# Performance work log

Measured on AMD Instinct MI355X. Metric: run time of the kernel, lower is better.

## Reference

```python
import jax, jax.numpy as jnp
import numpy as np

B, L, D = 1, 1024, 1024
NL = 4            # n_layers
N = 16            # d_state
DI = 2 * D        # d_inner (expand=2)
DTR = (D + 15) // 16  # dt_rank = ceil(d_model/16) = 64
K = 4             # depthwise conv kernel size
EPS = 1e-5


def setup_inputs() -> dict:
    key = jax.random.key(0)
    ks = jax.random.split(key, 8)
    s = lambda k, shp, sc: jax.random.normal(k, shp, jnp.float32) * sc
    x = s(ks[0], (B, L, D), 1.0)
    norm_w = jnp.ones((NL, D), jnp.float32)
    in_w = s(ks[1], (NL, 2 * DI, D), D ** -0.5)          # in_proj (no bias)
    conv_w = s(ks[2], (NL, DI, K), 0.5)                   # depthwise conv1d weight
    conv_b = s(ks[3], (NL, DI), 0.02)                     # conv1d bias
    xproj_w = s(ks[4], (NL, DTR + 2 * N, DI), DI ** -0.5) # x_proj (no bias)
    dt_w = s(ks[5], (NL, DI, DTR), DTR ** -0.5)           # dt_proj weight
    dt_b = jnp.full((NL, DI), 0.1, jnp.float32)           # dt_proj bias (positive-ish delta)
    A_log = jnp.log(jnp.tile(jnp.arange(1, N + 1, dtype=jnp.float32), (NL, DI, 1)))  # [NL, DI, N]
    D_skip = jnp.ones((NL, DI), jnp.float32)
    out_w = s(ks[6], (NL, D, DI), DI ** -0.5)             # out_proj (no bias)
    return dict(x=x, norm_w=norm_w, in_w=in_w, conv_w=conv_w, conv_b=conv_b,
                xproj_w=xproj_w, dt_w=dt_w, dt_b=dt_b, A_log=A_log,
                D_skip=D_skip, out_w=out_w)


def _rmsnorm(x, w):
    return x * jax.lax.rsqrt(jnp.mean(x * x, axis=-1, keepdims=True) + EPS) * w


def _causal_depthwise_conv(u, w, b):
    # u: [B, L, DI], w: [DI, K], b: [DI]; causal (left pad K-1)
    up = jnp.pad(u, ((0, 0), (K - 1, 0), (0, 0)))
    y = b
    for k in range(K):
        y = y + up[:, k:k + L, :] * w[:, k]
    return y


def _selective_scan(dA, dBu, C):
    # dA, dBu: [B, L, DI, N]; C: [B, L, N]
    def step(h, inp):
        a, bu, c = inp
        h = a * h + bu                       # [B, DI, N]
        y = jnp.einsum('bdn,bn->bd', h, c)   # [B, DI]
        return h, y
    h0 = jnp.zeros((dA.shape[0], DI, N), dA.dtype)
    _, ys = jax.lax.scan(step, h0, (dA.transpose(1, 0, 2, 3),
                                    dBu.transpose(1, 0, 2, 3),
                                    C.transpose(1, 0, 2)))
    return ys.transpose(1, 0, 2)             # [B, L, DI]


def _mamba_block(x, p):
    norm_w, in_w, conv_w, conv_b, xproj_w, dt_w, dt_b, A_log, D_skip, out_w = p
    xn = _rmsnorm(x, norm_w)
    xz = jnp.einsum('bld,ed->ble', xn, in_w)             # [B, L, 2*DI]
    u, z = jnp.split(xz, 2, axis=-1)
    u = jax.nn.silu(_causal_depthwise_conv(u, conv_w, conv_b))
    x_dbl = jnp.einsum('bld,ed->ble', u, xproj_w)        # [B, L, DTR+2N]
    dt_r, Bt, Ct = jnp.split(x_dbl, [DTR, DTR + N], axis=-1)
    delta = jax.nn.softplus(jnp.einsum('blr,dr->bld', dt_r, dt_w) + dt_b)  # [B, L, DI]
    A = -jnp.exp(A_log)                                  # [DI, N]
    dA = jnp.exp(delta[..., None] * A)                   # [B, L, DI, N]
    dBu = delta[..., None] * Bt[:, :, None, :] * u[..., None]
    y = _selective_scan(dA, dBu, Ct) + u * D_skip        # [B, L, DI]
    y = y * jax.nn.silu(z)
    return x + jnp.einsum('ble,de->bld', y, out_w)       # residual


def reference(x, norm_w, in_w, conv_w, conv_b, xproj_w, dt_w, dt_b, A_log, D_skip, out_w):
    params = (norm_w, in_w, conv_w, conv_b, xproj_w, dt_w, dt_b, A_log, D_skip, out_w)
    out, _ = jax.lax.scan(lambda h, p: (_mamba_block(h, p), None), x, params)
    return out
```

## Files before the change

kernel.cpp:

```cpp
#include <hip/hip_runtime.h>
#include <hip/hip_bf16.h>
#include <stdint.h>

#define L 1024
#define D 1024
#define NLAYER 4
#define NSTATE 16
#define DI 2048
#define DTR 64
#define KCONV 4
#define XD 96
#define NC 64
#define CT 16
#define KSPLIT 8
#define BK 32
#define DIST 4

typedef __attribute__((ext_vector_type(8))) short short8;
typedef __attribute__((ext_vector_type(4))) float floatx4;

__device__ __forceinline__ float siluf(float x) { return x / (1.f + __expf(-x)); }

__device__ __forceinline__ unsigned short f2bf(float x) {
    __hip_bfloat16 b = __float2bfloat16(x);
    return *reinterpret_cast<unsigned short*>(&b);
}

__device__ __forceinline__ short8 pack8(floatx4 a, floatx4 b) {
    short8 o;
    o[0] = (short)f2bf(a.x); o[1] = (short)f2bf(a.y);
    o[2] = (short)f2bf(a.z); o[3] = (short)f2bf(a.w);
    o[4] = (short)f2bf(b.x); o[5] = (short)f2bf(b.y);
    o[6] = (short)f2bf(b.z); o[7] = (short)f2bf(b.w);
    return o;
}

#define BARRIER_NODRAIN() asm volatile("s_waitcnt lgkmcnt(0)\n\ts_barrier" ::: "memory")

__global__ __launch_bounds__(256) void rmsnorm_kernel(const float* __restrict__ x,
                                                      const float* __restrict__ w,
                                                      __hip_bfloat16* __restrict__ out) {
    int row = blockIdx.x;
    const float* xr = x + (size_t)row * D;
    float v[4];
    float s = 0.f;
#pragma unroll
    for (int i = 0; i < 4; ++i) {
        v[i] = xr[threadIdx.x + i * 256];
        s += v[i] * v[i];
    }
#pragma unroll
    for (int off = 32; off > 0; off >>= 1) s += __shfl_xor(s, off, 64);
    __shared__ float red[4];
    int wave = threadIdx.x >> 6;
    if ((threadIdx.x & 63) == 0) red[wave] = s;
    __syncthreads();
    float tot = red[0] + red[1] + red[2] + red[3];
    float inv = rsqrtf(tot * (1.f / D) + 1e-5f);
#pragma unroll
    for (int i = 0; i < 4; ++i) {
        int c = threadIdx.x + i * 256;
        out[(size_t)row * D + c] = __float2bfloat16(v[i] * inv * w[c]);
    }
}

template <int EPI, int ITERS>
__global__ __launch_bounds__(256, 2) void gemm_pipe(
    const __hip_bfloat16* __restrict__ A, int lda,
    const float* __restrict__ Bw, int ldb, int Brows,
    float* __restrict__ C, int ldc, int Nvalid,
    long zstride, const float* __restrict__ bias) {
    __shared__ __align__(16) __hip_bfloat16 As[2][128 * BK];
    __shared__ __align__(16) __hip_bfloat16 Bs[2][64 * BK];
    int tid = threadIdx.x;
    int wave = tid >> 6, lane = tid & 63;

    int gxy = gridDim.x * gridDim.y;
    int total = gxy * gridDim.z;
    int flat = (blockIdx.z * gridDim.y + blockIdx.y) * gridDim.x + blockIdx.x;
    int bm, bn, bz;
    if ((total & 7) == 0) {
        int lid = (flat & 7) * (total >> 3) + (flat >> 3);
        bz = lid / gxy;
        int rem = lid - bz * gxy;
        bn = rem / gridDim.y;
        bm = rem - bn * gridDim.y;
    } else {
        bm = blockIdx.y; bn = blockIdx.x; bz = blockIdx.z;
    }

    int m0 = bm * 128, n0 = bn * 64;
    int k_base = bz * (ITERS * BK);
    C += (long)bz * zstride;
    int wr = wave >> 1, wc = wave & 1;
    int srow = lane >> 2, scol = (lane & 3) * 8;
    int q = lane >> 4, r = lane & 15;

    floatx4 acc[4][2] = {};

    const __hip_bfloat16* gA0 = A + (long)(m0 + wave * 32 + srow) * lda + scol + k_base;
    const __hip_bfloat16* gA1 = gA0 + (long)16 * lda;
    int bnrow = n0 + wave * 16 + srow;
    const float* gB = Bw + (long)bnrow * ldb + scol + k_base;
    bool bok = bnrow < Brows;

    short8 qa0[DIST], qa1[DIST];
    floatx4 qb0[DIST] = {}, qb1[DIST] = {};

    auto ld = [&](int j) {
        int k0 = j * BK;
        int s = j & (DIST - 1);
        qa0[s] = *(const short8*)(gA0 + k0);
        qa1[s] = *(const short8*)(gA1 + k0);
        if (bok) {
            qb0[s] = *(const floatx4*)(gB + k0);
            qb1[s] = *(const floatx4*)(gB + k0 + 4);
        }
    };
    auto wrstage = [&](int j) {
        int p = j & 1, s = j & (DIST - 1);
        *(short8*)(&As[p][(wave * 32 + srow) * BK + scol]) = qa0[s];
        *(short8*)(&As[p][(wave * 32 + 16 + srow) * BK + scol]) = qa1[s];
        *(short8*)(&Bs[p][(wave * 16 + srow) * BK + scol]) = pack8(qb0[s], qb1[s]);
    };

#pragma unroll
    for (int j = 0; j < DIST; ++j)
        if (j < ITERS) ld(j);
    wrstage(0);

#pragma unroll
    for (int k = 0; k < ITERS; ++k) {
        BARRIER_NODRAIN();
        if (k + DIST < ITERS) ld(k + DIST);
        if (k + 1 < ITERS) wrstage(k + 1);
        const short* Ap = (const short*)As[k & 1];
        const short* Bp = (const short*)Bs[k & 1];
        short8 af[4], bfr[2];
#pragma unroll
        for (int i = 0; i < 4; ++i)
            af[i] = *(const short8*)(Ap + (wr * 64 + i * 16 + r) * BK + q * 8);
#pragma unroll
        for (int j = 0; j < 2; ++j)
            bfr[j] = *(const short8*)(Bp + (wc * 32 + j * 16 + r) * BK + q * 8);
#pragma unroll
        for (int i = 0; i < 4; ++i)
#pragma unroll
            for (int j = 0; j < 2; ++j)
                acc[i][j] = __builtin_amdgcn_mfma_f32_16x16x32_bf16(af[i], bfr[j], acc[i][j], 0, 0, 0);
    }

#pragma unroll
    for (int i = 0; i < 4; ++i) {
        int mrow = m0 + wr * 64 + i * 16 + q * 4;
#pragma unroll
        for (int j = 0; j < 2; ++j) {
            int ncol = n0 + wc * 32 + j * 16 + r;
            if (ncol < Nvalid) {
#pragma unroll
                for (int rr = 0; rr < 4; ++rr) {
                    float v = acc[i][j][rr];
                    int m = mrow + rr;
                    if (EPI == 1) {
                        v += bias[ncol];
                        v = v > 20.f ? v : log1pf(__expf(v));
                    }
                    C[(long)m * ldc + ncol] = v;
                }
            }
        }
    }
}

template <bool NORM>
__global__ __launch_bounds__(256) void reduce2_kernel(const float* __restrict__ part2,
                                                      const float* __restrict__ xin,
                                                      const float* __restrict__ nw,
                                                      float* __restrict__ out,
                                                      __hip_bfloat16* __restrict__ xn) {
    int row = blockIdx.x;
    const float* p0 = part2 + (size_t)row * D;
    const float* p1 = p0 + (size_t)L * D;
    const float* xr = xin + (size_t)row * D;
    float v[4];
    float ss = 0.f;
#pragma unroll
    for (int i = 0; i < 4; ++i) {
        int c = threadIdx.x + i * 256;
        v[i] = p0[c] + p1[c] + xr[c];
        out[(size_t)row * D + c] = v[i];
        ss += v[i] * v[i];
    }
    if (NORM) {
#pragma unroll
        for (int off = 32; off > 0; off >>= 1) ss += __shfl_xor(ss, off, 64);
        __shared__ float red[4];
        int wave = threadIdx.x >> 6;
        if ((threadIdx.x & 63) == 0) red[wave] = ss;
        __syncthreads();
        float inv = rsqrtf((red[0] + red[1] + red[2] + red[3]) * (1.f / D) + 1e-5f);
#pragma unroll
        for (int i = 0; i < 4; ++i) {
            int c = threadIdx.x + i * 256;
            xn[(size_t)row * D + c] = __float2bfloat16(v[i] * inv * nw[c]);
        }
    }
}

__global__ __launch_bounds__(256) void conv_silu_kernel(const float* __restrict__ xz,
                                                        const float* __restrict__ cw,
                                                        const float* __restrict__ cb,
                                                        __hip_bfloat16* __restrict__ u) {
    int idx = blockIdx.x * 256 + threadIdx.x;
    int d = idx & (DI - 1);
    int t = idx >> 11;
    float acc = cb[d];
#pragma unroll
    for (int k = 0; k < KCONV; ++k) {
        int tk = t - (KCONV - 1) + k;
        if (tk >= 0) acc += xz[(size_t)tk * (2 * DI) + d] * cw[d * KCONV + k];
    }
    u[idx] = __float2bfloat16(siluf(acc));
}

__global__ __launch_bounds__(256) void xred_kernel(const float* __restrict__ part,
                                                   __hip_bfloat16* __restrict__ xdbl_bf,
                                                   float* __restrict__ xdblBC) {
    int i = blockIdx.x * 256 + threadIdx.x;
    int t = i / XD, col = i - t * XD;
    float s = 0.f;
#pragma unroll
    for (int sp = 0; sp < KSPLIT; ++sp) s += part[(size_t)sp * L * XD + i];
    if (col < DTR) xdbl_bf[(size_t)t * DTR + col] = __float2bfloat16(s);
    else xdblBC[(size_t)t * 32 + (col - DTR)] = s;
}

__global__ __launch_bounds__(256) void scanA_kernel(const float* __restrict__ delta,
                                                    const __hip_bfloat16* __restrict__ u,
                                                    const float* __restrict__ xdblBC,
                                                    const float* __restrict__ Alog,
                                                    float* __restrict__ Ach,
                                                    float* __restrict__ Bch) {
    int d = blockIdx.x * 256 + threadIdx.x;
    int c = blockIdx.y;
    __shared__ __align__(16) float Bsh[CT * NSTATE];
    int tt0 = threadIdx.x >> 4, c0 = threadIdx.x & 15;
    Bsh[threadIdx.x] = xdblBC[(size_t)(c * CT + tt0) * 32 + c0];
    __syncthreads();

    float aval[NSTATE];
    const float4* Al4 = (const float4*)(Alog + (size_t)d * NSTATE);
#pragma unroll
    for (int n4 = 0; n4 < 4; ++n4) {
        float4 t = Al4[n4];
        aval[n4 * 4 + 0] = -__expf(t.x);
        aval[n4 * 4 + 1] = -__expf(t.y);
        aval[n4 * 4 + 2] = -__expf(t.z);
        aval[n4 * 4 + 3] = -__expf(t.w);
    }
    float h[NSTATE], ap[NSTATE];
#pragma unroll
    for (int n = 0; n < NSTATE; ++n) { h[n] = 0.f; ap[n] = 1.f; }

    for (int tt = 0; tt < CT; ++tt) {
        int t = c * CT + tt;
        float dl = delta[(size_t)t * DI + d];
        float uu = __bfloat162float(u[(size_t)t * DI + d]);
        float du = dl * uu;
        const float4* Bv = (const float4*)(Bsh + tt * NSTATE);
#pragma unroll
        for (int n4 = 0; n4 < 4; ++n4) {
            float4 b = Bv[n4];
            float bb[4] = {b.x, b.y, b.z, b.w};
#pragma unroll
            for (int k = 0; k < 4; ++k) {
                int n = n4 * 4 + k;
                float a = __expf(dl * aval[n]);
                h[n] = a * h[n] + du * bb[k];
                ap[n] *= a;
            }
        }
    }
    float4* Ao = (float4*)(Ach + ((size_t)c * DI + d) * NSTATE);
    float4* Bo = (float4*)(Bch + ((size_t)c * DI + d) * NSTATE);
#pragma unroll
    for (int n4 = 0; n4 < 4; ++n4) {
        Ao[n4] = make_float4(ap[n4 * 4], ap[n4 * 4 + 1], ap[n4 * 4 + 2], ap[n4 * 4 + 3]);
        Bo[n4] = make_float4(h[n4 * 4], h[n4 * 4 + 1], h[n4 * 4 + 2], h[n4 * 4 + 3]);
    }
}

__global__ __launch_bounds__(256) void scanB_kernel(float* __restrict__ Ach,
                                                    const float* __restrict__ Bch) {
    long i = blockIdx.x * 256 + threadIdx.x;
    const long S = (long)DI * NSTATE;
    float h = 0.f;
    for (int c = 0; c < NC; ++c) {
        float a = Ach[c * S + i];
        float b = Bch[c * S + i];
        Ach[c * S + i] = h;
        h = a * h + b;
    }
}

__global__ __launch_bounds__(256) void scanC_kernel(const float* __restrict__ delta,
                                                    const __hip_bfloat16* __restrict__ u,
                                                    const float* __restrict__ xdblBC,
                                                    const float* __restrict__ Alog,
                                                    const float* __restrict__ Hin,
                                                    const float* __restrict__ xz,
                                                    const float* __restrict__ Dskip,
                                                    __hip_bfloat16* __restrict__ yg) {
    int d = blockIdx.x * 256 + threadIdx.x;
    int c = blockIdx.y;
    __shared__ __align__(16) float Bsh[CT * NSTATE];
    __shared__ __align__(16) float Csh[CT * NSTATE];
    int tt0 = threadIdx.x >> 4, c0 = threadIdx.x & 15;
    Bsh[threadIdx.x] = xdblBC[(size_t)(c * CT + tt0) * 32 + c0];
    Csh[threadIdx.x] = xdblBC[(size_t)(c * CT + tt0) * 32 + 16 + c0];
    __syncthreads();

    float aval[NSTATE];
    const float4* Al4 = (const float4*)(Alog + (size_t)d * NSTATE);
#pragma unroll
    for (int n4 = 0; n4 < 4; ++n4) {
        float4 t = Al4[n4];
        aval[n4 * 4 + 0] = -__expf(t.x);
        aval[n4 * 4 + 1] = -__expf(t.y);
        aval[n4 * 4 + 2] = -__expf(t.z);
        aval[n4 * 4 + 3] = -__expf(t.w);
    }
    float h[NSTATE];
    const float4* Hi = (const float4*)(Hin + ((size_t)c * DI + d) * NSTATE);
#pragma unroll
    for (int n4 = 0; n4 < 4; ++n4) {
        float4 t = Hi[n4];
        h[n4 * 4 + 0] = t.x; h[n4 * 4 + 1] = t.y; h[n4 * 4 + 2] = t.z; h[n4 * 4 + 3] = t.w;
    }
    float dsk = Dskip[d];

    for (int tt = 0; tt < CT; ++tt) {
        int t = c * CT + tt;
        float dl = delta[(size_t)t * DI + d];
        float uu = __bfloat162float(u[(size_t)t * DI + d]);
        float du = dl * uu;
        const float4* Bv = (const float4*)(Bsh + tt * NSTATE);
        const float4* Cv = (const float4*)(Csh + tt * NSTATE);
        float y = 0.f;
#pragma unroll
        for (int n4 = 0; n4 < 4; ++n4) {
            float4 b = Bv[n4];
            float4 cc = Cv[n4];
            float bb[4] = {b.x, b.y, b.z, b.w};
            float cv[4] = {cc.x, cc.y, cc.z, cc.w};
#pragma unroll
            for (int k = 0; k < 4; ++k) {
                int n = n4 * 4 + k;
                float a = __expf(dl * aval[n]);
                h[n] = a * h[n] + du * bb[k];
                y += h[n] * cv[k];
            }
        }
        float z = xz[(size_t)t * (2 * DI) + DI + d];
        yg[(size_t)t * DI + d] = __float2bfloat16((y + uu * dsk) * siluf(z));
    }
}

extern "C" void kernel_launch(void* const* d_in, const int* in_sizes, int n_in,
                              void* d_out, int out_size, void* d_ws, size_t ws_size,
                              hipStream_t stream) {
    const float* x      = (const float*)d_in[0];
    const float* norm_w = (const float*)d_in[1];
    const float* in_w   = (const float*)d_in[2];
    const float* conv_w = (const float*)d_in[3];
    const float* conv_b = (const float*)d_in[4];
    const float* xproj_w= (const float*)d_in[5];
    const float* dt_w   = (const float*)d_in[6];
    const float* dt_b   = (const float*)d_in[7];
    const float* A_log  = (const float*)d_in[8];
    const float* D_skip = (const float*)d_in[9];
    const float* out_w  = (const float*)d_in[10];
    float* out = (float*)d_out;

    uint8_t* wp = (uint8_t*)d_ws;
    auto alloc = [&](size_t bytes) {
        uint8_t* p = wp;
        wp += (bytes + 255) & ~(size_t)255;
        return p;
    };
    __hip_bfloat16* xn_bf   = (__hip_bfloat16*)alloc((size_t)L * D * 2);
    float*          xz      = (float*)alloc((size_t)L * 2 * DI * 4);
    __hip_bfloat16* u_bf    = (__hip_bfloat16*)alloc((size_t)L * DI * 2);
    float*          part    = (float*)alloc((size_t)KSPLIT * L * XD * 4);
    __hip_bfloat16* xdbl_bf = (__hip_bfloat16*)alloc((size_t)L * DTR * 2);
    float*          xdblBC  = (float*)alloc((size_t)L * 32 * 4);
    float*          delta   = (float*)alloc((size_t)L * DI * 4);
    __hip_bfloat16* yg_bf   = (__hip_bfloat16*)alloc((size_t)L * DI * 2);
    float*          part2   = (float*)alloc((size_t)2 * L * D * 4);
    float*          Ach     = (float*)alloc((size_t)NC * DI * NSTATE * 4);
    float*          Bch     = (float*)alloc((size_t)NC * DI * NSTATE * 4);

    rmsnorm_kernel<<<L, 256, 0, stream>>>(x, norm_w, xn_bf);

    for (int l = 0; l < NLAYER; ++l) {
        const float* xin = (l == 0) ? x : out;

        gemm_pipe<0, 32><<<dim3(4096 / 64, L / 128, 1), 256, 0, stream>>>(
            xn_bf, D, in_w + (size_t)l * 4096 * 1024, D, 4096,
            xz, 4096, 4096, 0, nullptr);

        conv_silu_kernel<<<L * DI / 256, 256, 0, stream>>>(
            xz, conv_w + (size_t)l * DI * KCONV, conv_b + (size_t)l * DI, u_bf);

        gemm_pipe<0, 8><<<dim3(2, L / 128, KSPLIT), 256, 0, stream>>>(
            u_bf, DI, xproj_w + (size_t)l * 96 * 2048, DI, 96,
            part, XD, XD, (long)L * XD, nullptr);
        xred_kernel<<<(L * XD) / 256, 256, 0, stream>>>(part, xdbl_bf, xdblBC);

        gemm_pipe<1, 2><<<dim3(2048 / 64, L / 128, 1), 256, 0, stream>>>(
            xdbl_bf, DTR, dt_w + (size_t)l * 2048 * 64, DTR, 2048,
            delta, DI, DI, 0, dt_b + (size_t)l * DI);

        scanA_kernel<<<dim3(DI / 256, NC), 256, 0, stream>>>(
            delta, u_bf, xdblBC, A_log + (size_t)l * DI * NSTATE, Ach, Bch);
        scanB_kernel<<<(DI * NSTATE) / 256, 256, 0, stream>>>(Ach, Bch);
        scanC_kernel<<<dim3(DI / 256, NC), 256, 0, stream>>>(
            delta, u_bf, xdblBC, A_log + (size_t)l * DI * NSTATE, Ach, xz,
            D_skip + (size_t)l * DI, yg_bf);

        gemm_pipe<0, 32><<<dim3(1024 / 64, L / 128, 2), 256, 0, stream>>>(
            yg_bf, DI, out_w + (size_t)l * 1024 * 2048, DI, 1024,
            part2, D, D, (long)L * D, nullptr);

        if (l < NLAYER - 1)
            reduce2_kernel<true><<<L, 256, 0, stream>>>(
                part2, xin, norm_w + (size_t)(l + 1) * D, out, xn_bf);
        else
            reduce2_kernel<false><<<L, 256, 0, stream>>>(
                part2, xin, nullptr, out, nullptr);
    }
}
```

Baseline: 608.4 us.

## Use 128x128 tile GEMM for in/out projections and prefetch chunk-scan loads

Adds a gemm128 kernel with 128x128 output tiles, 4x4 MFMA per wave and an XCD-aware block remap. It replaces the 64-wide tile GEMM for in_proj and out_proj to raise operand reuse. out_proj now splits K four ways, and the reduce kernel is generalised to sum a variable number of partials. scanB now preloads eight chunks ahead to hide its serial global load latency. The costs are more partial-sum traffic to reduce, higher register pressure, and fewer blocks for in_proj (256).

```diff
diff --git a/kernel.cpp b/kernel.cpp
--- a/kernel.cpp
+++ b/kernel.cpp
@@ -13,6 +13,7 @@
 #define NC 64
 #define CT 16
 #define KSPLIT 8
+#define OSPLIT 4
 #define BK 32
 #define DIST 4
 
@@ -172,24 +173,131 @@
     }
 }
 
-template <bool NORM>
-__global__ __launch_bounds__(256) void reduce2_kernel(const float* __restrict__ part2,
-                                                      const float* __restrict__ xin,
-                                                      const float* __restrict__ nw,
-                                                      float* __restrict__ out,
-                                                      __hip_bfloat16* __restrict__ xn) {
+template <int ITERS>
+__global__ __launch_bounds__(256, 1) void gemm128(
+    const __hip_bfloat16* __restrict__ A, int lda,
+    const float* __restrict__ Bw, int ldb, int Brows,
+    float* __restrict__ C, int ldc,
+    long zstride) {
+    __shared__ __align__(16) __hip_bfloat16 As[2][128 * BK];
+    __shared__ __align__(16) __hip_bfloat16 Bs[2][128 * BK];
+    int tid = threadIdx.x;
+    int wave = tid >> 6, lane = tid & 63;
+
+    int gxy = gridDim.x * gridDim.y;
+    int total = gxy * gridDim.z;
+    int flat = (blockIdx.z * gridDim.y + blockIdx.y) * gridDim.x + blockIdx.x;
+    int bm, bn, bz;
+    if ((total & 7) == 0) {
+        int lid = (flat & 7) * (total >> 3) + (flat >> 3);
+        bz = lid / gxy;
+        int rem = lid - bz * gxy;
+        bn = rem / gridDim.y;
+        bm = rem - bn * gridDim.y;
+    } else {
+        bm = blockIdx.y; bn = blockIdx.x; bz = blockIdx.z;
+    }
+
+    int m0 = bm * 128, n0 = bn * 128;
+    int k_base = bz * (ITERS * BK);
+    C += (long)bz * zstride;
+    int wr = wave >> 1, wc = wave & 1;
+    int srow = lane >> 2, scol = (lane & 3) * 8;
+    int q = lane >> 4, r = lane & 15;
+
+    floatx4 acc[4][4] = {};
+
+    const __hip_bfloat16* gA0 = A + (long)(m0 + wave * 32 + srow) * lda + scol + k_base;
+    const __hip_bfloat16* gA1 = gA0 + (long)16 * lda;
+    int bn0 = n0 + wave * 32 + srow;
+    const float* gB0 = Bw + (long)bn0 * ldb + scol + k_base;
+    const float* gB1 = gB0 + (long)16 * ldb;
+    bool bok0 = bn0 < Brows, bok1 = (bn0 + 16) < Brows;
+
+    short8 qa0[DIST], qa1[DIST];
+    floatx4 qb0[DIST] = {}, qb1[DIST] = {}, qb2[DIST] = {}, qb3[DIST] = {};
+
+    auto ld = [&](int j) {
+        int k0 = j * BK;
+        int s = j & (DIST - 1);
+        qa0[s] = *(const short8*)(gA0 + k0);
+        qa1[s] = *(const short8*)(gA1 + k0);
+        if (bok0) {
+            qb0[s] = *(const floatx4*)(gB0 + k0);
+            qb1[s] = *(const floatx4*)(gB0 + k0 + 4);
+        }
+        if (bok1) {
+            qb2[s] = *(const floatx4*)(gB1 + k0);
+            qb3[s] = *(const floatx4*)(gB1 + k0 + 4);
+        }
+    };
+    auto wrstage = [&](int j) {
+        int p = j & 1, s = j & (DIST - 1);
+        *(short8*)(&As[p][(wave * 32 + srow) * BK + scol]) = qa0[s];
+        *(short8*)(&As[p][(wave * 32 + 16 + srow) * BK + scol]) = qa1[s];
+        *(short8*)(&Bs[p][(wave * 32 + srow) * BK + scol]) = pack8(qb0[s], qb1[s]);
+        *(short8*)(&Bs[p][(wave * 32 + 16 + srow) * BK + scol]) = pack8(qb2[s], qb3[s]);
+    };
+
+#pragma unroll
+    for (int j = 0; j < DIST; ++j)
+        if (j < ITERS) ld(j);
+    wrstage(0);
+
+#pragma unroll
+    for (int k = 0; k < ITERS; ++k) {
+        BARRIER_NODRAIN();
+        if (k + DIST < ITERS) ld(k + DIST);
+        if (k + 1 < ITERS) wrstage(k + 1);
+        const short* Ap = (const short*)As[k & 1];
+        const short* Bp = (const short*)Bs[k & 1];
+        short8 af[4], bfr[4];
+#pragma unroll
+        for (int i = 0; i < 4; ++i)
+            af[i] = *(const short8*)(Ap + (wr * 64 + i * 16 + r) * BK + q * 8);
+#pragma unroll
+        for (int j = 0; j < 4; ++j)
+            bfr[j] = *(const short8*)(Bp + (wc * 64 + j * 16 + r) * BK + q * 8);
+#pragma unroll
+        for (int i = 0; i < 4; ++i)
+#pragma unroll
+            for (int j = 0; j < 4; ++j)
+                acc[i][j] = __builtin_amdgcn_mfma_f32_16x16x32_bf16(af[i], bfr[j], acc[i][j], 0, 0, 0);
+    }
+
+#pragma unroll
+    for (int i = 0; i < 4; ++i) {
+        int mrow = m0 + wr * 64 + i * 16 + q * 4;
+#pragma unroll
+        for (int j = 0; j < 4; ++j) {
+            int ncol = n0 + wc * 64 + j * 16 + r;
+#pragma unroll
+            for (int rr = 0; rr < 4; ++rr)
+                C[(long)(mrow + rr) * ldc + ncol] = acc[i][j][rr];
+        }
+    }
+}
+
+template <int NPART, bool NORM>
+__global__ __launch_bounds__(256) void reduce_kernel(const float* __restrict__ part2,
+                                                     const float* __restrict__ xin,
+                                                     const float* __restrict__ nw,
+                                                     float* __restrict__ out,
+                                                     __hip_bfloat16* __restrict__ xn) {
     int row = blockIdx.x;
-    const float* p0 = part2 + (size_t)row * D;
-    const float* p1 = p0 + (size_t)L * D;
     const float* xr = xin + (size_t)row * D;
     float v[4];
     float ss = 0.f;
 #pragma unroll
     for (int i = 0; i < 4; ++i) {
         int c = threadIdx.x + i * 256;
-        v[i] = p0[c] + p1[c] + xr[c];
-        out[(size_t)row * D + c] = v[i];
-        ss += v[i] * v[i];
+        float s = xr[c];
+#pragma unroll
+        for (int p = 0; p < NPART; ++p)
+            s += part2[(size_t)p * L * D + (size_t)row * D + c];
+        v[i] = s;
+        out[(size_t)row * D + c] = s;
+        ss += s * s;
     }
     if (NORM) {
 #pragma unroll
@@ -294,11 +402,23 @@
                                                     const float* __restrict__ Bch) {
     long i = blockIdx.x * 256 + threadIdx.x;
     const long S = (long)DI * NSTATE;
+    constexpr int P = 8;
+    float ab[P], bb[P];
+#pragma unroll
+    for (int j = 0; j < P; ++j) {
+        ab[j] = Ach[(long)j * S + i];
+        bb[j] = Bch[(long)j * S + i];
+    }
     float h = 0.f;
+#pragma unroll
     for (int c = 0; c < NC; ++c) {
-        float a = Ach[c * S + i];
-        float b = Bch[c * S + i];
-        Ach[c * S + i] = h;
+        float a = ab[c & (P - 1)];
+        float b = bb[c & (P - 1)];
+        Ach[(long)c * S + i] = h;
+        if (c + P < NC) {
+            ab[c & (P - 1)] = Ach[(long)(c + P) * S + i];
+            bb[c & (P - 1)] = Bch[(long)(c + P) * S + i];
+        }
         h = a * h + b;
     }
 }
@@ -396,7 +516,7 @@
     float*          xdblBC  = (float*)alloc((size_t)L * 32 * 4);
     float*          delta   = (float*)alloc((size_t)L * DI * 4);
     __hip_bfloat16* yg_bf   = (__hip_bfloat16*)alloc((size_t)L * DI * 2);
-    float*          part2   = (float*)alloc((size_t)2 * L * D * 4);
+    float*          part2   = (float*)alloc((size_t)OSPLIT * L * D * 4);
     float*          Ach     = (float*)alloc((size_t)NC * DI * NSTATE * 4);
     float*          Bch     = (float*)alloc((size_t)NC * DI * NSTATE * 4);
 
@@ -405,9 +525,9 @@
     for (int l = 0; l < NLAYER; ++l) {
         const float* xin = (l == 0) ? x : out;
 
-        gemm_pipe<0, 32><<<dim3(4096 / 64, L / 128, 1), 256, 0, stream>>>(
+        gemm128<32><<<dim3(4096 / 128, L / 128, 1), 256, 0, stream>>>(
             xn_bf, D, in_w + (size_t)l * 4096 * 1024, D, 4096,
-            xz, 4096, 4096, 0, nullptr);
+            xz, 4096, 0);
 
         conv_silu_kernel<<<L * DI / 256, 256, 0, stream>>>(
             xz, conv_w + (size_t)l * DI * KCONV, conv_b + (size_t)l * DI, u_bf);
@@ -428,15 +548,15 @@
             delta, u_bf, xdblBC, A_log + (size_t)l * DI * NSTATE, Ach, xz,
             D_skip + (size_t)l * DI, yg_bf);
 
-        gemm_pipe<0, 32><<<dim3(1024 / 64, L / 128, 2), 256, 0, stream>>>(
+        gemm128<16><<<dim3(1024 / 128, L / 128, OSPLIT), 256, 0, stream>>>(
             yg_bf, DI, out_w + (size_t)l * 1024 * 2048, DI, 1024,
-            part2, D, D, (long)L * D, nullptr);
+            part2, D, (long)L * D);
 
         if (l < NLAYER - 1)
-            reduce2_kernel<true><<<L, 256, 0, stream>>>(
+            reduce_kernel<OSPLIT, true><<<L, 256, 0, stream>>>(
                 part2, xin, norm_w + (size_t)(l + 1) * D, out, xn_bf);
         else
-            reduce2_kernel<false><<<L, 256, 0, stream>>>(
+            reduce_kernel<OSPLIT, false><<<L, 256, 0, stream>>>(
                 part2, xin, nullptr, out, nullptr);
     }
 }
```

After: 598.7 us. About the same (-1.6%).
